# Kernel optimization log

Measured on AMD Instinct MI355X. Metric: run time of the kernel, lower is better.

Reference implementation:

```python
import jax, jax.numpy as jnp
import numpy as np

B, L = 4, 256
N1 = N2 = PD = 64
D, K, O = 8, 6, 64          # n_detectors, n_anchors_per_detector, n_outputs
A = 1 << K                  # LUT size per detector = 64
F = N1 + N2 + PD            # triple width = 192


def setup_inputs() -> dict:
    key = jax.random.key(0)
    k1, k2, k3, k4, k5 = jax.random.split(key, 5)
    input_1 = jax.random.normal(k1, (B, L, N1), dtype=jnp.float32)
    input_2 = jax.random.normal(k2, (B, L, N2), dtype=jnp.float32)
    # positional table sized L so index j-i in [1, L-1] is valid
    pos_emb = jax.random.uniform(k3, (L, PD), dtype=jnp.float32, minval=-1.0, maxval=1.0)
    # inner LUTLayer params: anchor hyperplanes and per-address LUT weights
    anchors = jax.random.normal(k4, (D, K, F), dtype=jnp.float32) / np.float32(np.sqrt(F))
    lut_weights = jax.random.normal(k5, (D, A, O), dtype=jnp.float32) * 0.05
    return {"input_1": input_1, "input_2": input_2, "pos_emb": pos_emb,
            "anchors": anchors, "lut_weights": lut_weights}


def _pair_indices(L):
    i_idx, j_idx = np.triu_indices(L, k=1)  # all pairs i < j, P = L*(L-1)/2
    return jnp.asarray(i_idx, jnp.int32), jnp.asarray(j_idx, jnp.int32)


_CODES = jnp.asarray(((np.arange(1 << K)[:, None] >> np.arange(K)) & 1).astype(np.float32))  # [A, K]


def _lut_forward(x, anchors, lut_weights):
    # x: [B, P, F] -> [B, P, O]; soft LUT: per-detector anchor bits -> address distribution -> LUT read
    logits = jnp.einsum('bpf,dkf->bpdk', x, anchors)            # [B,P,D,K]
    la = jax.nn.log_sigmoid(logits)                              # log p(bit=1)
    lb = jax.nn.log_sigmoid(-logits)                             # log p(bit=0)
    logp = jnp.einsum('bpdk,ak->bpda', la, _CODES) + jnp.einsum('bpdk,ak->bpda', lb, 1.0 - _CODES)
    prob = jnp.exp(logp)                                         # [B,P,D,A]
    return jnp.einsum('bpda,dao->bpo', prob, lut_weights)        # sum over detectors


def reference(input_1, input_2, pos_emb, anchors, lut_weights):
    Lq = input_1.shape[1]
    i_idx, j_idx = _pair_indices(Lq)
    # gather the O(L^2) triples in one pass: [B, P, F]
    x = jnp.concatenate([input_1[:, i_idx, :],
                         input_2[:, j_idx, :],
                         jnp.broadcast_to(pos_emb[j_idx - i_idx][None], (input_1.shape[0], i_idx.shape[0], PD))],
                        axis=-1)
    pair_out = _lut_forward(x, anchors, lut_weights)             # [B, P, O]
    # sum pairs into their target position j (position 0 has no pairs -> zeros)
    Pn = pair_out.shape[1]
    flat = pair_out.swapaxes(0, 1).reshape(Pn, -1)               # [P, B*O]
    seg = jax.ops.segment_sum(flat, j_idx, num_segments=Lq)      # [L, B*O]
    return seg.reshape(Lq, pair_out.shape[0], O).swapaxes(0, 1)  # [B, L, O]
```

## Files before the change

kernel.cpp:

```cpp
#include <hip/hip_runtime.h>
#include <hip/hip_bf16.h>

#define BB 4
#define LL 256
#define N1 64
#define DD 8
#define KK 6
#define OO 64
#define AA 64
#define FF 192
#define DK 48

__device__ float g_T1[BB * LL * DK];
__device__ float g_T3[BB * LL * DK];
__device__ float g_T2[LL * DK];

__global__ __launch_bounds__(64) void precompute_logits(
    const float* __restrict__ in1, const float* __restrict__ in2,
    const float* __restrict__ pos, const float* __restrict__ anchors) {
  const int r = blockIdx.x;
  const int t = threadIdx.x;
  const float* src;
  float* dst;
  int off;
  if (r < BB * LL) {
    src = in1 + r * N1;        dst = g_T1 + r * DK;        off = 0;
  } else if (r < 2 * BB * LL) {
    const int q = r - BB * LL;
    src = in2 + q * N1;        dst = g_T3 + q * DK;        off = 64;
  } else {
    const int q = r - 2 * BB * LL;
    src = pos + q * N1;        dst = g_T2 + q * DK;        off = 128;
  }
  __shared__ float x[64];
  x[t] = src[t];
  __syncthreads();
  if (t < DK) {
    const float* av = anchors + t * FF + off;
    float s = 0.f;
#pragma unroll
    for (int f = 0; f < 64; ++f) s = fmaf(x[f], av[f], s);
    dst[t] = s;
  }
}

__global__ __launch_bounds__(256, 3) void lut_pairs_kernel(
    const float* __restrict__ lutw, float* __restrict__ out) {
  const int tid  = threadIdx.x;
  const int lane = tid & 63;
  const int wv   = tid >> 6;
  const int bj   = blockIdx.x;
  const int j    = bj & (LL - 1);
  const int b    = bj >> 8;

  __shared__ float q[4 * 512];
  __shared__ float red[256];

#pragma unroll
  for (int t = 0; t < 8; ++t) q[tid + t * 256] = 0.f;
  __syncthreads();

  if (wv * 64 < j) {
    const int i     = wv * 64 + lane;
    const bool act  = i < j;
    const int ic    = act ? i : 0;
    const int delta = j - ic;

    float l[DK];
    {
      const float4* p1 = (const float4*)(g_T1 + (b * LL + ic) * DK);
      const float4* p2 = (const float4*)(g_T2 + delta * DK);
      const float4* p3 = (const float4*)(g_T3 + (b * LL + j) * DK);
#pragma unroll
      for (int t = 0; t < 12; ++t) {
        const float4 a = p1[t], c = p2[t], e = p3[t];
        l[4 * t + 0] = a.x + c.x + e.x;
        l[4 * t + 1] = a.y + c.y + e.y;
        l[4 * t + 2] = a.z + c.z + e.z;
        l[4 * t + 3] = a.w + c.w + e.w;
      }
    }

    const float base = act ? 1.f : 0.f;

#pragma unroll 1
    for (int d = 0; d < DD; ++d) {
      float F0[KK], F1[KK];
#pragma unroll
      for (int k = 0; k < KK; ++k) {
        const float lg = l[d * KK + k];
        const float s1 = __fdividef(1.f, 1.f + __expf(-lg));
        const float s0 = 1.f - s1;
        const bool bk  = (lane >> k) & 1;
        F1[k] = bk ? s0 : s1;
        F0[k] = bk ? s1 : s0;
      }
      float cur[AA];
      cur[0] = base;
#pragma unroll
      for (int k = 0; k < KK; ++k) {
        const int sz = 1 << k;
#pragma unroll
        for (int m = 0; m < sz; ++m) {
          cur[m + sz] = cur[m] * F1[k];
          cur[m]      = cur[m] * F0[k];
        }
      }
#pragma unroll
      for (int k = 0; k < KK; ++k) {
        const int st = 1 << k;
#pragma unroll
        for (int m = 0; m < AA; m += 2 * st)
          cur[m] += __shfl_xor(cur[m + st], st);
      }
      q[wv * 512 + d * 64 + lane] = cur[0];
    }
  }
  __syncthreads();

#pragma unroll
  for (int t = 0; t < 2; ++t) {
    const int s = tid + t * 256;
    q[s] = q[s] + q[512 + s] + q[1024 + s] + q[1536 + s];
  }
  __syncthreads();

  float acc = 0.f;
  const float* wq = lutw + (wv * 128) * OO + lane;
#pragma unroll 4
  for (int s = 0; s < 128; ++s)
    acc = fmaf(q[wv * 128 + s], wq[s * OO], acc);
  red[tid] = acc;
  __syncthreads();
  if (tid < OO)
    out[bj * OO + tid] = red[tid] + red[64 + tid] + red[128 + tid] + red[192 + tid];
}

extern "C" void kernel_launch(void* const* d_in, const int* in_sizes, int n_in,
                              void* d_out, int out_size, void* d_ws, size_t ws_size,
                              hipStream_t stream) {
  const float* in1  = (const float*)d_in[0];
  const float* in2  = (const float*)d_in[1];
  const float* pos  = (const float*)d_in[2];
  const float* anc  = (const float*)d_in[3];
  const float* lutw = (const float*)d_in[4];
  float* out = (float*)d_out;

  precompute_logits<<<2 * BB * LL + LL, 64, 0, stream>>>(in1, in2, pos, anc);
  lut_pairs_kernel<<<BB * LL, 256, 0, stream>>>(lutw, out);
}
```

Before: 108.4 us.

## Batch rows per block in logit precompute and stream logits per detector

Result: faster. 96.42 us (-11.0%).

```diff
diff --git a/kernel.cpp b/kernel.cpp
--- a/kernel.cpp
+++ b/kernel.cpp
@@ -11,36 +11,53 @@
 #define FF 192
 #define DK 48
 
-__device__ float g_T1[BB * LL * DK];
-__device__ float g_T3[BB * LL * DK];
-__device__ float g_T2[LL * DK];
+#define R1 1024
+#define R2 256
+#define RPB 5
+#define NB1 205
+#define NB2 52
 
-__global__ __launch_bounds__(64) void precompute_logits(
+__device__ float g_T1[R1 * DK];
+__device__ float g_T3[R1 * DK];
+__device__ float g_T2[R2 * DK];
+
+__global__ __launch_bounds__(256) void precompute_logits(
     const float* __restrict__ in1, const float* __restrict__ in2,
     const float* __restrict__ pos, const float* __restrict__ anchors) {
-  const int r = blockIdx.x;
-  const int t = threadIdx.x;
+  const int bid = blockIdx.x;
+  const int tid = threadIdx.x;
   const float* src;
   float* dst;
-  int off;
-  if (r < BB * LL) {
-    src = in1 + r * N1;        dst = g_T1 + r * DK;        off = 0;
-  } else if (r < 2 * BB * LL) {
-    const int q = r - BB * LL;
-    src = in2 + q * N1;        dst = g_T3 + q * DK;        off = 64;
+  int off, row0, nrows;
+  if (bid < NB1) {
+    src = in1; dst = g_T1; off = 0;   row0 = bid * RPB;             nrows = R1;
+  } else if (bid < 2 * NB1) {
+    src = in2; dst = g_T3; off = 64;  row0 = (bid - NB1) * RPB;     nrows = R1;
   } else {
-    const int q = r - 2 * BB * LL;
-    src = pos + q * N1;        dst = g_T2 + q * DK;        off = 128;
+    src = pos; dst = g_T2; off = 128; row0 = (bid - 2 * NB1) * RPB; nrows = R2;
   }
-  __shared__ float x[64];
-  x[t] = src[t];
+
+  __shared__ float as[DK * 65];
+  __shared__ float xs[RPB * 64];
+#pragma unroll
+  for (int idx = tid; idx < DK * 64; idx += 256) {
+    const int dk = idx >> 6, f = idx & 63;
+    as[dk * 65 + f] = anchors[dk * FF + off + f];
+  }
+#pragma unroll
+  for (int idx = tid; idx < RPB * 64; idx += 256) {
+    const int rl = idx >> 6, f = idx & 63, r = row0 + rl;
+    xs[idx] = (r < nrows) ? src[r * 64 + f] : 0.f;
+  }
   __syncthreads();
-  if (t < DK) {
-    const float* av = anchors + t * FF + off;
-    float s = 0.f;
+
+  if (tid < RPB * DK) {
+    const int rl = tid / DK, dk = tid - rl * DK, r = row0 + rl;
+    float acc = 0.f;
 #pragma unroll
-    for (int f = 0; f < 64; ++f) s = fmaf(x[f], av[f], s);
-    dst[t] = s;
+    for (int f = 0; f < 64; ++f)
+      acc = fmaf(xs[rl * 64 + f], as[dk * 65 + f], acc);
+    if (r < nrows) dst[r * DK + dk] = acc;
   }
 }
 
@@ -53,9 +70,11 @@
   const int j    = bj & (LL - 1);
   const int b    = bj >> 8;
 
+  __shared__ float l3[DK];
   __shared__ float q[4 * 512];
   __shared__ float red[256];
 
+  if (tid < DK) l3[tid] = g_T3[bj * DK + tid];
 #pragma unroll
   for (int t = 0; t < 8; ++t) q[tid + t * 256] = 0.f;
   __syncthreads();
@@ -66,30 +85,30 @@
     const int ic    = act ? i : 0;
     const int delta = j - ic;
 
-    float l[DK];
-    {
-      const float4* p1 = (const float4*)(g_T1 + (b * LL + ic) * DK);
-      const float4* p2 = (const float4*)(g_T2 + delta * DK);
-      const float4* p3 = (const float4*)(g_T3 + (b * LL + j) * DK);
-#pragma unroll
-      for (int t = 0; t < 12; ++t) {
-        const float4 a = p1[t], c = p2[t], e = p3[t];
-        l[4 * t + 0] = a.x + c.x + e.x;
-        l[4 * t + 1] = a.y + c.y + e.y;
-        l[4 * t + 2] = a.z + c.z + e.z;
-        l[4 * t + 3] = a.w + c.w + e.w;
-      }
-    }
-
+    const float* r1 = g_T1 + (b * LL + ic) * DK;
+    const float* r2 = g_T2 + delta * DK;
     const float base = act ? 1.f : 0.f;
 
 #pragma unroll 1
     for (int d = 0; d < DD; ++d) {
+      const float2 a0 = *(const float2*)(r1 + d * KK + 0);
+      const float2 a1 = *(const float2*)(r1 + d * KK + 2);
+      const float2 a2 = *(const float2*)(r1 + d * KK + 4);
+      const float2 c0 = *(const float2*)(r2 + d * KK + 0);
+      const float2 c1 = *(const float2*)(r2 + d * KK + 2);
+      const float2 c2 = *(const float2*)(r2 + d * KK + 4);
+      float lg[KK];
+      lg[0] = a0.x + c0.x + l3[d * KK + 0];
+      lg[1] = a0.y + c0.y + l3[d * KK + 1];
+      lg[2] = a1.x + c1.x + l3[d * KK + 2];
+      lg[3] = a1.y + c1.y + l3[d * KK + 3];
+      lg[4] = a2.x + c2.x + l3[d * KK + 4];
+      lg[5] = a2.y + c2.y + l3[d * KK + 5];
+
       float F0[KK], F1[KK];
 #pragma unroll
       for (int k = 0; k < KK; ++k) {
-        const float lg = l[d * KK + k];
-        const float s1 = __fdividef(1.f, 1.f + __expf(-lg));
+        const float s1 = __fdividef(1.f, 1.f + __expf(-lg[k]));
         const float s0 = 1.f - s1;
         const bool bk  = (lane >> k) & 1;
         F1[k] = bk ? s0 : s1;
@@ -146,6 +165,6 @@
   const float* lutw = (const float*)d_in[4];
   float* out = (float*)d_out;
 
-  precompute_logits<<<2 * BB * LL + LL, 64, 0, stream>>>(in1, in2, pos, anc);
+  precompute_logits<<<2 * NB1 + NB2, 256, 0, stream>>>(in1, in2, pos, anc);
   lut_pairs_kernel<<<BB * LL, 256, 0, stream>>>(lutw, out);
 }
```
